# Performance work log

Hardware: AMD Instinct MI355X
Metric: run time of the kernel (lower is better)

The kernel has to match this reference:

```python
import jax, jax.numpy as jnp
import numpy as np

N_NODES = 50000
N_EDGES = 800000
N_GRAPHS = 256
N_FEAT, N_HID, N_EMB = 128, 256, 256
BN_EPS = 1e-5
W_SCALE = 0.05  # keep activations well-scaled through 3 layers


def setup_inputs() -> dict:
    key = jax.random.key(0)
    ks = jax.random.split(key, 9)
    x = jax.random.normal(ks[0], (N_NODES, N_FEAT), jnp.float32)
    edge_index = jax.random.randint(ks[1], (2, N_EDGES), 0, N_NODES)
    batch = jnp.sort(jax.random.randint(ks[2], (N_NODES,), 0, N_GRAPHS))
    return {
        "x": x,
        "edge_index": edge_index,
        "batch": batch,
        "W1_0": jax.random.normal(ks[3], (N_FEAT, N_HID), jnp.float32) * W_SCALE,
        "W2_0": jax.random.normal(ks[4], (N_HID, N_HID), jnp.float32) * W_SCALE,
        "gamma0": jnp.ones((N_HID,), jnp.float32),
        "beta0": jnp.zeros((N_HID,), jnp.float32),
        "W1_1": jax.random.normal(ks[5], (N_HID, N_HID), jnp.float32) * W_SCALE,
        "W2_1": jax.random.normal(ks[6], (N_HID, N_HID), jnp.float32) * W_SCALE,
        "gamma1": jnp.ones((N_HID,), jnp.float32),
        "beta1": jnp.zeros((N_HID,), jnp.float32),
        "W1_2": jax.random.normal(ks[7], (N_HID, N_HID), jnp.float32) * W_SCALE,
        "W2_2": jax.random.normal(ks[8], (N_HID, N_EMB), jnp.float32) * W_SCALE,
    }


def _gin_conv(x, src, dst, W1, W2):
    # PyG GINConv, eps=0: nn((1+eps)*x_i + sum_{j in N(i)} x_j)
    agg = jax.ops.segment_sum(x[src], dst, num_segments=N_NODES)  # [N, d]
    h = x + agg
    return jax.nn.relu(h @ W1) @ W2  # Linear(bias=False) -> act -> Linear(bias=False)


def _batch_norm(h, gamma, beta):
    # BatchNorm1d in training mode: biased batch stats over nodes
    mean = jnp.mean(h, axis=0)
    var = jnp.var(h, axis=0)
    return (h - mean) * jax.lax.rsqrt(var + BN_EPS) * gamma + beta


def reference(x, edge_index, batch, W1_0, W2_0, gamma0, beta0,
              W1_1, W2_1, gamma1, beta1, W1_2, W2_2):
    src, dst = edge_index[0], edge_index[1]
    layers = [(W1_0, W2_0, gamma0, beta0), (W1_1, W2_1, gamma1, beta1)]
    xs = []
    h = x
    for W1, W2, g, b in layers:  # n_layers-1 conv+act+BN blocks
        h = jax.nn.relu(_gin_conv(h, src, dst, W1, W2))
        h = _batch_norm(h, g, b)
        xs.append(h)
    h = _gin_conv(h, src, dst, W1_2, W2_2)  # final conv: no act, no BN
    xs.append(h)
    xpool = jax.ops.segment_sum(h, batch, num_segments=N_GRAPHS)  # global_add_pool
    return xpool, jnp.concatenate(xs, axis=1)
```

## Files before the change

### kernel.cpp

```cpp
#include <hip/hip_runtime.h>
#include <stdint.h>

typedef unsigned int u32;
typedef unsigned short u16;

using s16x8 = __attribute__((ext_vector_type(8))) short;
using f32x4 = __attribute__((ext_vector_type(4))) float;

#define N_NODES_C 50000
#define N_EDGES_C 800000
#define N_GRAPHS_C 256
#define N_FEAT_C 128
#define N_HID_C 256

static __device__ __forceinline__ float bf2f(u16 u) {
  union { u32 u; float f; } c; c.u = ((u32)u) << 16; return c.f;
}
static __device__ __forceinline__ u16 f2bf(float f) {
  union { float f; u32 u; } c; c.f = f;
  u32 u = c.u;
  return (u16)((u + 0x7fffu + ((u >> 16) & 1u)) >> 16);
}

static __device__ __forceinline__ void gload_lds16(const u16* g, u16* l) {
  __builtin_amdgcn_global_load_lds(
      (const __attribute__((address_space(1))) unsigned int*)g,
      (__attribute__((address_space(3))) unsigned int*)l, 16, 0, 0);
}

__global__ void convt_all_kernel(const float* __restrict__ Wa, const float* __restrict__ Wb,
                                 const float* __restrict__ Wc, const float* __restrict__ Wd,
                                 const float* __restrict__ We, const float* __restrict__ Wf,
                                 u16* oa, u16* ob, u16* oc, u16* od, u16* oe, u16* of_) {
  int m = blockIdx.y;
  const float* W; u16* o; int K;
  switch (m) {
    case 0: W = Wa; o = oa; K = 128; break;
    case 1: W = Wb; o = ob; K = 256; break;
    case 2: W = Wc; o = oc; K = 256; break;
    case 3: W = Wd; o = od; K = 256; break;
    case 4: W = We; o = oe; K = 256; break;
    default: W = Wf; o = of_; K = 256; break;
  }
  int idx = blockIdx.x * 256 + threadIdx.x;
  if (idx >= K * 256) return;
  int n = idx / K, k = idx - n * K;
  o[idx] = f2bf(W[(size_t)k * 256 + n]);
}

__global__ void cvt_kernel(const float* __restrict__ x, u16* __restrict__ xb, int n) {
  int idx = blockIdx.x * 256 + threadIdx.x;
  if (idx < n) xb[idx] = f2bf(x[idx]);
}

__global__ void count_kernel(const int* __restrict__ dst, int* __restrict__ cnt, int E) {
  int e = blockIdx.x * 256 + threadIdx.x;
  if (e < E) atomicAdd(&cnt[dst[e]], 1);
}

__global__ void scanA_kernel(const int* __restrict__ cnt, int* __restrict__ incl,
                             int* __restrict__ bsum, int n) {
  __shared__ int sd[1024];
  int i = blockIdx.x * 1024 + (int)threadIdx.x;
  int v = (i < n) ? cnt[i] : 0;
  sd[threadIdx.x] = v;
  __syncthreads();
  for (int off = 1; off < 1024; off <<= 1) {
    int t = ((int)threadIdx.x >= off) ? sd[threadIdx.x - off] : 0;
    __syncthreads();
    sd[threadIdx.x] += t;
    __syncthreads();
  }
  if (i < n) incl[i] = sd[threadIdx.x];
  if (threadIdx.x == 1023) bsum[blockIdx.x] = sd[1023];
}

__global__ void scanB_kernel(int* bsum, int nb) {
  if (threadIdx.x == 0) {
    int s = 0;
    for (int b = 0; b < nb; b++) { int t = bsum[b]; bsum[b] = s; s += t; }
  }
}

__global__ void scanC_kernel(const int* __restrict__ cnt, const int* __restrict__ incl,
                             const int* __restrict__ bsum, int* __restrict__ offs,
                             int* __restrict__ cursor, int n) {
  int i = blockIdx.x * 1024 + (int)threadIdx.x;
  if (i < n) {
    int e = incl[i] - cnt[i] + bsum[blockIdx.x];
    offs[i] = e;
    cursor[i] = e;
  }
  if (i == 0) offs[n] = N_EDGES_C;
}

__global__ void fill_kernel(const int* __restrict__ src, const int* __restrict__ dst,
                            int* __restrict__ cursor, int* __restrict__ csr, int E) {
  int e = blockIdx.x * 256 + threadIdx.x;
  if (e < E) {
    int p = atomicAdd(&cursor[dst[e]], 1);
    csr[p] = src[e];
  }
}

template <int D>
__global__ __launch_bounds__(256) void agg_kernel(const u16* __restrict__ xin,
                                                  const int* __restrict__ offs,
                                                  const int* __restrict__ csr,
                                                  u16* __restrict__ hout) {
  constexpr int LPE = D / 8;
  constexpr int EPW = 64 / LPE;
  int wid = threadIdx.x >> 6, lane = threadIdx.x & 63;
  int node = blockIdx.x * 4 + wid;
  if (node >= N_NODES_C) return;
  int sub = lane / LPE;
  int fl = lane % LPE;
  int f0 = fl * 8;
  float acc[8];
  if (sub == 0) {
    uint4 v = *reinterpret_cast<const uint4*>(xin + (size_t)node * D + f0);
    const u32* pv = reinterpret_cast<const u32*>(&v);
#pragma unroll
    for (int t = 0; t < 4; t++) {
      acc[2 * t] = bf2f((u16)pv[t]);
      acc[2 * t + 1] = bf2f((u16)(pv[t] >> 16));
    }
  } else {
#pragma unroll
    for (int t = 0; t < 8; t++) acc[t] = 0.f;
  }
  int e1 = offs[node + 1];
  for (int e = offs[node] + sub; e < e1; e += EPW) {
    int s = csr[e];
    uint4 v = *reinterpret_cast<const uint4*>(xin + (size_t)s * D + f0);
    const u32* pv = reinterpret_cast<const u32*>(&v);
#pragma unroll
    for (int t = 0; t < 4; t++) {
      acc[2 * t] += bf2f((u16)pv[t]);
      acc[2 * t + 1] += bf2f((u16)(pv[t] >> 16));
    }
  }
#pragma unroll
  for (int j = 0; j < 8; j++) {
    if (EPW == 4) acc[j] += __shfl_xor(acc[j], 16, 64);
    acc[j] += __shfl_xor(acc[j], 32, 64);
  }
  if (sub == 0) {
    u32 w[4];
#pragma unroll
    for (int t = 0; t < 4; t++)
      w[t] = (u32)f2bf(acc[2 * t]) | ((u32)f2bf(acc[2 * t + 1]) << 16);
    *reinterpret_cast<uint4*>(hout + (size_t)node * D + f0) =
        *reinterpret_cast<const uint4*>(w);
  }
}

template <int K, bool RELU, bool OUTF32, bool STATS>
__global__ __launch_bounds__(256) void gemm_kernel(const u16* __restrict__ A,
                                                   const u16* __restrict__ Bt,
                                                   u16* __restrict__ outB,
                                                   float* __restrict__ outF, int ldc,
                                                   float* __restrict__ statsp) {
  constexpr int BM = 128, BN = 128, BK = 64;
  __shared__ u16 Al[BM * BK];
  __shared__ u16 Bl[BN * BK];
  const int tid = threadIdx.x;
  const int wid = tid >> 6, lane = tid & 63;
  const int brow = blockIdx.x * BM;
  const int bcol = blockIdx.y * BN;
  const int wr = (wid >> 1) * 64, wc = (wid & 1) * 64;
  f32x4 acc[4][4] = {};

  const int lrow = lane >> 3;
  const int lw = lane & 7;
  const int colA = ((lw ^ lrow) * 8);
  const int sw = (lane & 7) << 3;

  for (int k0 = 0; k0 < K; k0 += BK) {
#pragma unroll
    for (int i = 0; i < 4; i++) {
      int c = wid * 4 + i;
      int r = c * 8 + lrow;
      int gr = brow + r;
      gr = gr < N_NODES_C ? gr : N_NODES_C - 1;
      gload_lds16(A + (size_t)gr * K + k0 + colA, &Al[c * 512]);
      gload_lds16(Bt + (size_t)(bcol + r) * K + k0 + colA, &Bl[c * 512]);
    }
    __syncthreads();
#pragma unroll
    for (int ks = 0; ks < BK; ks += 32) {
      const int kk = ks + (lane >> 4) * 8;
      const int ki = kk ^ sw;
      s16x8 a[4], b[4];
#pragma unroll
      for (int m = 0; m < 4; m++)
        a[m] = *reinterpret_cast<const s16x8*>(&Al[(wr + m * 16 + (lane & 15)) * 64 + ki]);
#pragma unroll
      for (int n = 0; n < 4; n++)
        b[n] = *reinterpret_cast<const s16x8*>(&Bl[(wc + n * 16 + (lane & 15)) * 64 + ki]);
#pragma unroll
      for (int m = 0; m < 4; m++)
#pragma unroll
        for (int n = 0; n < 4; n++)
          acc[m][n] = __builtin_amdgcn_mfma_f32_16x16x32_bf16(a[m], b[n], acc[m][n], 0, 0, 0);
    }
    __syncthreads();
  }

  const int cb = bcol + wc + (lane & 15);
  const int rsub = (lane >> 4) * 4;
  float s1[4] = {0.f, 0.f, 0.f, 0.f}, s2[4] = {0.f, 0.f, 0.f, 0.f};
#pragma unroll
  for (int m = 0; m < 4; m++) {
#pragma unroll
    for (int r = 0; r < 4; r++) {
      int row = brow + wr + m * 16 + rsub + r;
      if (row >= N_NODES_C) continue;
#pragma unroll
      for (int n = 0; n < 4; n++) {
        float v = acc[m][n][r];
        if (RELU) v = v > 0.f ? v : 0.f;
        int col = cb + n * 16;
        if (OUTF32)
          outF[(size_t)row * ldc + col] = v;
        else
          outB[(size_t)row * ldc + col] = f2bf(v);
        if (STATS) { s1[n] += v; s2[n] += v * v; }
      }
    }
  }
  if (STATS) {
#pragma unroll
    for (int n = 0; n < 4; n++) {
      float a0 = s1[n], b0 = s2[n];
      a0 += __shfl_xor(a0, 16, 64);
      b0 += __shfl_xor(b0, 16, 64);
      a0 += __shfl_xor(a0, 32, 64);
      b0 += __shfl_xor(b0, 32, 64);
      if (lane < 16) {
        atomicAdd(&statsp[cb + n * 16], a0);
        atomicAdd(&statsp[256 + cb + n * 16], b0);
      }
    }
  }
}

__global__ void scalebias_kernel(const float* __restrict__ stats, const float* __restrict__ gamma,
                                 const float* __restrict__ beta, float* __restrict__ sb) {
  int f = threadIdx.x;
  const float invM = 1.0f / (float)N_NODES_C;
  float mean = stats[f] * invM;
  float var = stats[256 + f] * invM - mean * mean;
  float sc = gamma[f] * rsqrtf(var + 1e-5f);
  sb[f] = sc;
  sb[256 + f] = beta[f] - mean * sc;
}

__global__ __launch_bounds__(256) void norm_kernel(float* __restrict__ c, int ldc,
                                                   const float* __restrict__ sb,
                                                   u16* __restrict__ xn) {
  int f = threadIdx.x;
  float sc = sb[f], bi = sb[256 + f];
  for (int r = blockIdx.x; r < N_NODES_C; r += gridDim.x) {
    size_t idx = (size_t)r * ldc + f;
    float y = fmaf(c[idx], sc, bi);
    c[idx] = y;
    xn[(size_t)r * 256 + f] = f2bf(y);
  }
}

__global__ __launch_bounds__(256) void pool_kernel(const float* __restrict__ c, int ldc,
                                                   const int* __restrict__ batch,
                                                   float* __restrict__ outp) {
  __shared__ float red[1024];
  int g = blockIdx.x;
  int wid = threadIdx.x >> 6, lane = threadIdx.x & 63;
  int lo = 0, hi = N_NODES_C;
  while (lo < hi) { int mid = (lo + hi) >> 1; if (batch[mid] < g) lo = mid + 1; else hi = mid; }
  int start = lo;
  hi = N_NODES_C;
  while (lo < hi) { int mid = (lo + hi) >> 1; if (batch[mid] <= g) lo = mid + 1; else hi = mid; }
  int end = lo;
  float acc[4] = {0.f, 0.f, 0.f, 0.f};
  for (int r = start + wid; r < end; r += 4) {
    float4 v = *reinterpret_cast<const float4*>(c + (size_t)r * ldc + lane * 4);
    acc[0] += v.x; acc[1] += v.y; acc[2] += v.z; acc[3] += v.w;
  }
#pragma unroll
  for (int j = 0; j < 4; j++) red[wid * 256 + lane * 4 + j] = acc[j];
  __syncthreads();
  int f = threadIdx.x;
  float s = red[f] + red[256 + f] + red[512 + f] + red[768 + f];
  outp[(size_t)g * 256 + f] = s;
}

extern "C" void kernel_launch(void* const* d_in, const int* in_sizes, int n_in,
                              void* d_out, int out_size, void* d_ws, size_t ws_size,
                              hipStream_t stream) {
  (void)in_sizes; (void)n_in; (void)out_size; (void)ws_size;
  const float* x = (const float*)d_in[0];
  const int* ei = (const int*)d_in[1];
  const int* batch = (const int*)d_in[2];
  const float* W1_0 = (const float*)d_in[3];
  const float* W2_0 = (const float*)d_in[4];
  const float* gamma0 = (const float*)d_in[5];
  const float* beta0 = (const float*)d_in[6];
  const float* W1_1 = (const float*)d_in[7];
  const float* W2_1 = (const float*)d_in[8];
  const float* gamma1 = (const float*)d_in[9];
  const float* beta1 = (const float*)d_in[10];
  const float* W1_2 = (const float*)d_in[11];
  const float* W2_2 = (const float*)d_in[12];

  float* out = (float*)d_out;
  float* xpool = out;
  float* concat = out + (size_t)N_GRAPHS_C * N_HID_C;

  char* ws = (char*)d_ws;
  size_t off = 0;
  auto alloc = [&](size_t bytes) -> char* {
    char* p = ws + off;
    off = (off + bytes + 255) & ~(size_t)255;
    return p;
  };
  int* cnt = (int*)alloc((N_NODES_C + 1) * 4);
  int* offs = (int*)alloc((N_NODES_C + 1) * 4);
  int* cursor = (int*)alloc(N_NODES_C * 4);
  int* incl = (int*)alloc(N_NODES_C * 4);
  int* bsum = (int*)alloc(64 * 4);
  int* csr = (int*)alloc((size_t)N_EDGES_C * 4);
  u16* xb = (u16*)alloc((size_t)N_NODES_C * N_FEAT_C * 2);
  u16* hin = (u16*)alloc((size_t)N_NODES_C * N_HID_C * 2);
  u16* tbuf = (u16*)alloc((size_t)N_NODES_C * N_HID_C * 2);
  u16* xn = (u16*)alloc((size_t)N_NODES_C * N_HID_C * 2);
  u16* w10t = (u16*)alloc((size_t)N_FEAT_C * N_HID_C * 2);
  u16* w20t = (u16*)alloc((size_t)N_HID_C * N_HID_C * 2);
  u16* w11t = (u16*)alloc((size_t)N_HID_C * N_HID_C * 2);
  u16* w21t = (u16*)alloc((size_t)N_HID_C * N_HID_C * 2);
  u16* w12t = (u16*)alloc((size_t)N_HID_C * N_HID_C * 2);
  u16* w22t = (u16*)alloc((size_t)N_HID_C * N_HID_C * 2);
  float* stats = (float*)alloc(512 * 4);
  float* sb = (float*)alloc(512 * 4);

  const int* srcv = ei;
  const int* dstv = ei + N_EDGES_C;
  const int nb = (N_NODES_C + 1023) / 1024;

  hipMemsetAsync(cnt, 0, (N_NODES_C + 1) * 4, stream);

  convt_all_kernel<<<dim3(256, 6), 256, 0, stream>>>(W1_0, W2_0, W1_1, W2_1, W1_2, W2_2,
                                                     w10t, w20t, w11t, w21t, w12t, w22t);
  cvt_kernel<<<(N_NODES_C * N_FEAT_C + 255) / 256, 256, 0, stream>>>(x, xb, N_NODES_C * N_FEAT_C);

  count_kernel<<<(N_EDGES_C + 255) / 256, 256, 0, stream>>>(dstv, cnt, N_EDGES_C);
  scanA_kernel<<<nb, 1024, 0, stream>>>(cnt, incl, bsum, N_NODES_C);
  scanB_kernel<<<1, 64, 0, stream>>>(bsum, nb);
  scanC_kernel<<<nb, 1024, 0, stream>>>(cnt, incl, bsum, offs, cursor, N_NODES_C);
  fill_kernel<<<(N_EDGES_C + 255) / 256, 256, 0, stream>>>(srcv, dstv, cursor, csr, N_EDGES_C);

  dim3 ggrid((N_NODES_C + 127) / 128, 2);

  agg_kernel<128><<<(N_NODES_C + 3) / 4, 256, 0, stream>>>(xb, offs, csr, hin);
  gemm_kernel<128, true, false, false><<<ggrid, 256, 0, stream>>>(hin, w10t, tbuf, nullptr, N_HID_C, nullptr);
  hipMemsetAsync(stats, 0, 512 * 4, stream);
  gemm_kernel<256, true, true, true><<<ggrid, 256, 0, stream>>>(tbuf, w20t, nullptr, concat + 0, 768, stats);
  scalebias_kernel<<<1, 256, 0, stream>>>(stats, gamma0, beta0, sb);
  norm_kernel<<<2048, 256, 0, stream>>>(concat + 0, 768, sb, xn);

  agg_kernel<256><<<(N_NODES_C + 3) / 4, 256, 0, stream>>>(xn, offs, csr, hin);
  gemm_kernel<256, true, false, false><<<ggrid, 256, 0, stream>>>(hin, w11t, tbuf, nullptr, N_HID_C, nullptr);
  hipMemsetAsync(stats, 0, 512 * 4, stream);
  gemm_kernel<256, true, true, true><<<ggrid, 256, 0, stream>>>(tbuf, w21t, nullptr, concat + 256, 768, stats);
  scalebias_kernel<<<1, 256, 0, stream>>>(stats, gamma1, beta1, sb);
  norm_kernel<<<2048, 256, 0, stream>>>(concat + 256, 768, sb, xn);

  agg_kernel<256><<<(N_NODES_C + 3) / 4, 256, 0, stream>>>(xn, offs, csr, hin);
  gemm_kernel<256, true, false, false><<<ggrid, 256, 0, stream>>>(hin, w12t, tbuf, nullptr, N_HID_C, nullptr);
  gemm_kernel<256, false, true, false><<<ggrid, 256, 0, stream>>>(tbuf, w22t, nullptr, concat + 512, 768, nullptr);

  pool_kernel<<<N_GRAPHS_C, 256, 0, stream>>>(concat + 512, 768, batch, xpool);
}
```

Measured before the change: 498.9 us.

## Widen GEMM tiles to full N, fuse BN scale into norm, vectorize cvt and agg

The GEMM now runs 512-thread blocks that cover all 256 output columns per 128-row tile. This drops the 2-way column grid, so A tiles are loaded once rather than twice. The BN-stat GEMMs now write bf16 into a scratch buffer instead of fp32 into concat. The norm kernel computes scale and bias itself, reads the bf16, and writes both the fp32 concat slice and the bf16 next-layer input, which removes the scalebias launch and the fp32 read-modify-write. Also included are a float4-vectorized input conversion and a 2-way unrolled edge loop in aggregation. One side effect is that the fp32 concat output is now normalized from bf16-rounded pre-BN values, which slightly lowers precision.

```diff
diff --git a/kernel.cpp b/kernel.cpp
--- a/kernel.cpp
+++ b/kernel.cpp
@@ -48,9 +48,14 @@
   o[idx] = f2bf(W[(size_t)k * 256 + n]);
 }
 
-__global__ void cvt_kernel(const float* __restrict__ x, u16* __restrict__ xb, int n) {
+__global__ void cvt4_kernel(const float* __restrict__ x, u16* __restrict__ xb, int n4) {
   int idx = blockIdx.x * 256 + threadIdx.x;
-  if (idx < n) xb[idx] = f2bf(x[idx]);
+  if (idx >= n4) return;
+  float4 v = reinterpret_cast<const float4*>(x)[idx];
+  u32 lo = (u32)f2bf(v.x) | ((u32)f2bf(v.y) << 16);
+  u32 hi = (u32)f2bf(v.z) | ((u32)f2bf(v.w) << 16);
+  uint2 w; w.x = lo; w.y = hi;
+  reinterpret_cast<uint2*>(xb)[idx] = w;
 }
 
 __global__ void count_kernel(const int* __restrict__ dst, int* __restrict__ cnt, int E) {
@@ -129,8 +134,22 @@
 #pragma unroll
     for (int t = 0; t < 8; t++) acc[t] = 0.f;
   }
+  int e = offs[node] + sub;
   int e1 = offs[node + 1];
-  for (int e = offs[node] + sub; e < e1; e += EPW) {
+  for (; e + EPW < e1; e += 2 * EPW) {
+    int s0 = csr[e];
+    int s1 = csr[e + EPW];
+    uint4 v0 = *reinterpret_cast<const uint4*>(xin + (size_t)s0 * D + f0);
+    uint4 v1 = *reinterpret_cast<const uint4*>(xin + (size_t)s1 * D + f0);
+    const u32* p0 = reinterpret_cast<const u32*>(&v0);
+    const u32* p1 = reinterpret_cast<const u32*>(&v1);
+#pragma unroll
+    for (int t = 0; t < 4; t++) {
+      acc[2 * t] += bf2f((u16)p0[t]) + bf2f((u16)p1[t]);
+      acc[2 * t + 1] += bf2f((u16)(p0[t] >> 16)) + bf2f((u16)(p1[t] >> 16));
+    }
+  }
+  if (e < e1) {
     int s = csr[e];
     uint4 v = *reinterpret_cast<const uint4*>(xin + (size_t)s * D + f0);
     const u32* pv = reinterpret_cast<const u32*>(&v);
@@ -156,35 +175,40 @@
 }
 
 template <int K, bool RELU, bool OUTF32, bool STATS>
-__global__ __launch_bounds__(256) void gemm_kernel(const u16* __restrict__ A,
-                                                   const u16* __restrict__ Bt,
-                                                   u16* __restrict__ outB,
-                                                   float* __restrict__ outF, int ldc,
-                                                   float* __restrict__ statsp) {
-  constexpr int BM = 128, BN = 128, BK = 64;
+__global__ __launch_bounds__(512, 2) void gemm_kernel(const u16* __restrict__ A,
+                                                      const u16* __restrict__ Bt,
+                                                      u16* __restrict__ outB,
+                                                      float* __restrict__ outF, int ldc,
+                                                      float* __restrict__ statsp) {
+  constexpr int BM = 128, BK = 64;
   __shared__ u16 Al[BM * BK];
-  __shared__ u16 Bl[BN * BK];
+  __shared__ u16 Bl[256 * BK];
   const int tid = threadIdx.x;
   const int wid = tid >> 6, lane = tid & 63;
   const int brow = blockIdx.x * BM;
-  const int bcol = blockIdx.y * BN;
-  const int wr = (wid >> 1) * 64, wc = (wid & 1) * 64;
+  const int wr = (wid >> 2) * 64;
+  const int wc = (wid & 3) * 64;
   f32x4 acc[4][4] = {};
 
   const int lrow = lane >> 3;
   const int lw = lane & 7;
-  const int colA = ((lw ^ lrow) * 8);
+  const int colA = (lw ^ lrow) * 8;
   const int sw = (lane & 7) << 3;
 
   for (int k0 = 0; k0 < K; k0 += BK) {
 #pragma unroll
-    for (int i = 0; i < 4; i++) {
-      int c = wid * 4 + i;
-      int r = c * 8 + lrow;
-      int gr = brow + r;
-      gr = gr < N_NODES_C ? gr : N_NODES_C - 1;
-      gload_lds16(A + (size_t)gr * K + k0 + colA, &Al[c * 512]);
-      gload_lds16(Bt + (size_t)(bcol + r) * K + k0 + colA, &Bl[c * 512]);
+    for (int i = 0; i < 6; i++) {
+      int c = wid * 6 + i;
+      if (c < 16) {
+        int r = c * 8 + lrow;
+        int gr = brow + r;
+        gr = gr < N_NODES_C ? gr : N_NODES_C - 1;
+        gload_lds16(A + (size_t)gr * K + k0 + colA, &Al[c * 512]);
+      } else {
+        int cc = c - 16;
+        int r = cc * 8 + lrow;
+        gload_lds16(Bt + (size_t)r * K + k0 + colA, &Bl[cc * 512]);
+      }
     }
     __syncthreads();
 #pragma unroll
@@ -207,7 +231,7 @@
     __syncthreads();
   }
 
-  const int cb = bcol + wc + (lane & 15);
+  const int cb = wc + (lane & 15);
   const int rsub = (lane >> 4) * 4;
   float s1[4] = {0.f, 0.f, 0.f, 0.f}, s2[4] = {0.f, 0.f, 0.f, 0.f};
 #pragma unroll
@@ -245,27 +269,30 @@
   }
 }
 
-__global__ void scalebias_kernel(const float* __restrict__ stats, const float* __restrict__ gamma,
-                                 const float* __restrict__ beta, float* __restrict__ sb) {
-  int f = threadIdx.x;
+__global__ __launch_bounds__(256) void norm_kernel(const u16* __restrict__ xp,
+                                                   const float* __restrict__ stats,
+                                                   const float* __restrict__ gamma,
+                                                   const float* __restrict__ beta,
+                                                   float* __restrict__ cout,
+                                                   u16* __restrict__ xn) {
   const float invM = 1.0f / (float)N_NODES_C;
-  float mean = stats[f] * invM;
-  float var = stats[256 + f] * invM - mean * mean;
-  float sc = gamma[f] * rsqrtf(var + 1e-5f);
-  sb[f] = sc;
-  sb[256 + f] = beta[f] - mean * sc;
-}
-
-__global__ __launch_bounds__(256) void norm_kernel(float* __restrict__ c, int ldc,
-                                                   const float* __restrict__ sb,
-                                                   u16* __restrict__ xn) {
-  int f = threadIdx.x;
-  float sc = sb[f], bi = sb[256 + f];
-  for (int r = blockIdx.x; r < N_NODES_C; r += gridDim.x) {
-    size_t idx = (size_t)r * ldc + f;
-    float y = fmaf(c[idx], sc, bi);
-    c[idx] = y;
-    xn[(size_t)r * 256 + f] = f2bf(y);
+  int f0 = (threadIdx.x & 127) * 2;
+  int half = threadIdx.x >> 7;
+  float m0 = stats[f0] * invM, m1 = stats[f0 + 1] * invM;
+  float v0 = stats[256 + f0] * invM - m0 * m0;
+  float v1 = stats[256 + f0 + 1] * invM - m1 * m1;
+  float sc0 = gamma[f0] * rsqrtf(v0 + 1e-5f);
+  float sc1 = gamma[f0 + 1] * rsqrtf(v1 + 1e-5f);
+  float bi0 = beta[f0] - m0 * sc0;
+  float bi1 = beta[f0 + 1] - m1 * sc1;
+  for (int r = blockIdx.x * 2 + half; r < N_NODES_C; r += 2 * gridDim.x) {
+    u32 w = *reinterpret_cast<const u32*>(xp + (size_t)r * 256 + f0);
+    float y0 = fmaf(bf2f((u16)w), sc0, bi0);
+    float y1 = fmaf(bf2f((u16)(w >> 16)), sc1, bi1);
+    float2 y; y.x = y0; y.y = y1;
+    *reinterpret_cast<float2*>(cout + (size_t)r * 768 + f0) = y;
+    *reinterpret_cast<u32*>(xn + (size_t)r * 256 + f0) =
+        (u32)f2bf(y0) | ((u32)f2bf(y1) << 16);
   }
 }
 
@@ -340,17 +367,18 @@
   u16* w12t = (u16*)alloc((size_t)N_HID_C * N_HID_C * 2);
   u16* w22t = (u16*)alloc((size_t)N_HID_C * N_HID_C * 2);
   float* stats = (float*)alloc(512 * 4);
-  float* sb = (float*)alloc(512 * 4);
 
   const int* srcv = ei;
   const int* dstv = ei + N_EDGES_C;
   const int nb = (N_NODES_C + 1023) / 1024;
+  const int ggrid = (N_NODES_C + 127) / 128;
 
   hipMemsetAsync(cnt, 0, (N_NODES_C + 1) * 4, stream);
 
   convt_all_kernel<<<dim3(256, 6), 256, 0, stream>>>(W1_0, W2_0, W1_1, W2_1, W1_2, W2_2,
                                                      w10t, w20t, w11t, w21t, w12t, w22t);
-  cvt_kernel<<<(N_NODES_C * N_FEAT_C + 255) / 256, 256, 0, stream>>>(x, xb, N_NODES_C * N_FEAT_C);
+  cvt4_kernel<<<(N_NODES_C * N_FEAT_C / 4 + 255) / 256, 256, 0, stream>>>(
+      x, xb, N_NODES_C * N_FEAT_C / 4);
 
   count_kernel<<<(N_EDGES_C + 255) / 256, 256, 0, stream>>>(dstv, cnt, N_EDGES_C);
   scanA_kernel<<<nb, 1024, 0, stream>>>(cnt, incl, bsum, N_NODES_C);
@@ -358,25 +386,21 @@
   scanC_kernel<<<nb, 1024, 0, stream>>>(cnt, incl, bsum, offs, cursor, N_NODES_C);
   fill_kernel<<<(N_EDGES_C + 255) / 256, 256, 0, stream>>>(srcv, dstv, cursor, csr, N_EDGES_C);
 
-  dim3 ggrid((N_NODES_C + 127) / 128, 2);
-
   agg_kernel<128><<<(N_NODES_C + 3) / 4, 256, 0, stream>>>(xb, offs, csr, hin);
-  gemm_kernel<128, true, false, false><<<ggrid, 256, 0, stream>>>(hin, w10t, tbuf, nullptr, N_HID_C, nullptr);
+  gemm_kernel<128, true, false, false><<<ggrid, 512, 0, stream>>>(hin, w10t, tbuf, nullptr, N_HID_C, nullptr);
   hipMemsetAsync(stats, 0, 512 * 4, stream);
-  gemm_kernel<256, true, true, true><<<ggrid, 256, 0, stream>>>(tbuf, w20t, nullptr, concat + 0, 768, stats);
-  scalebias_kernel<<<1, 256, 0, stream>>>(stats, gamma0, beta0, sb);
-  norm_kernel<<<2048, 256, 0, stream>>>(concat + 0, 768, sb, xn);
+  gemm_kernel<256, true, false, true><<<ggrid, 512, 0, stream>>>(tbuf, w20t, hin, nullptr, N_HID_C, stats);
+  norm_kernel<<<2048, 256, 0, stream>>>(hin, stats, gamma0, beta0, concat + 0, xn);
 
   agg_kernel<256><<<(N_NODES_C + 3) / 4, 256, 0, stream>>>(xn, offs, csr, hin);
-  gemm_kernel<256, true, false, false><<<ggrid, 256, 0, stream>>>(hin, w11t, tbuf, nullptr, N_HID_C, nullptr);
+  gemm_kernel<256, true, false, false><<<ggrid, 512, 0, stream>>>(hin, w11t, tbuf, nullptr, N_HID_C, nullptr);
   hipMemsetAsync(stats, 0, 512 * 4, stream);
-  gemm_kernel<256, true, true, true><<<ggrid, 256, 0, stream>>>(tbuf, w21t, nullptr, concat + 256, 768, stats);
-  scalebias_kernel<<<1, 256, 0, stream>>>(stats, gamma1, beta1, sb);
-  norm_kernel<<<2048, 256, 0, stream>>>(concat + 256, 768, sb, xn);
+  gemm_kernel<256, true, false, true><<<ggrid, 512, 0, stream>>>(tbuf, w21t, hin, nullptr, N_HID_C, stats);
+  norm_kernel<<<2048, 256, 0, stream>>>(hin, stats, gamma1, beta1, concat + 256, xn);
 
   agg_kernel<256><<<(N_NODES_C + 3) / 4, 256, 0, stream>>>(xn, offs, csr, hin);
-  gemm_kernel<256, true, false, false><<<ggrid, 256, 0, stream>>>(hin, w12t, tbuf, nullptr, N_HID_C, nullptr);
-  gemm_kernel<256, false, true, false><<<ggrid, 256, 0, stream>>>(tbuf, w22t, nullptr, concat + 512, 768, nullptr);
+  gemm_kernel<256, true, false, false><<<ggrid, 512, 0, stream>>>(hin, w12t, tbuf, nullptr, N_HID_C, nullptr);
+  gemm_kernel<256, false, true, false><<<ggrid, 512, 0, stream>>>(tbuf, w22t, nullptr, concat + 512, 768, nullptr);
 
   pool_kernel<<<N_GRAPHS_C, 256, 0, stream>>>(concat + 512, 768, batch, xpool);
 }
```

Result: faster. 467.5 us (-6.3%).
